# Kernel tuning notes

Hardware: AMD Instinct MI355X
Metric: run time of the kernel (lower is better)

Reference implementation:

```python
import jax, jax.numpy as jnp
import numpy as np


def setup_inputs() -> dict:
    key = jax.random.key(0)
    ks = jax.random.split(key, 5)
    B, T, C, HS = 8, 2048, 1024, 64
    return {
        "x_q": jax.random.normal(ks[0], (B, T, C), dtype=jnp.float32),
        "x_kv": jax.random.normal(ks[1], (B, T, C), dtype=jnp.float32),
        "Wq": jax.random.normal(ks[2], (C, HS), dtype=jnp.float32) * (C ** -0.5),
        "Wk": jax.random.normal(ks[3], (C, HS), dtype=jnp.float32) * (C ** -0.5),
        "Wv": jax.random.normal(ks[4], (C, HS), dtype=jnp.float32) * (C ** -0.5),
    }


def reference(x_q, x_kv, Wq, Wk, Wv):
    # x_q, x_kv: [B, T, C]; W*: [C, HS]
    B, T, C = x_q.shape
    q = jnp.einsum("btc,ch->bth", x_q, Wq)   # [B, T, HS]
    k = jnp.einsum("btc,ch->bth", x_kv, Wk)  # [B, T, HS]
    v = jnp.einsum("btc,ch->bth", x_kv, Wv)  # [B, T, HS]
    # NOTE: original scales by d_model**-0.5 (C), not head_size**-0.5
    wei = jnp.einsum("bqh,bkh->bqk", q, k) * (C ** -0.5)  # [B, T, T]
    causal = jnp.tril(jnp.ones((T, T), dtype=bool))
    wei = jnp.where(causal, wei, -jnp.inf)
    wei = jax.nn.softmax(wei, axis=-1)
    out = jnp.einsum("bqk,bkh->bqh", wei, v)  # [B, T, HS]
    return out
```

## Files before the change

### kernel.cpp

```cpp
#include <hip/hip_runtime.h>

typedef __bf16 bf16_t;
typedef __bf16 bf16x8 __attribute__((ext_vector_type(8)));
typedef float f32x4 __attribute__((ext_vector_type(4)));
typedef unsigned short u16x4 __attribute__((ext_vector_type(4)));

#define B_ 8
#define T_ 2048
#define C_ 1024
#define HS_ 64

#define MFMA __builtin_amdgcn_mfma_f32_16x16x32_bf16

__device__ __forceinline__ float fast_exp2(float x) {
#if __has_builtin(__builtin_amdgcn_exp2f)
  return __builtin_amdgcn_exp2f(x);
#else
  return exp2f(x);
#endif
}

__global__ __launch_bounds__(256) void repack_w(
    const float* __restrict__ Wq, const float* __restrict__ Wk,
    const float* __restrict__ Wv, bf16_t* __restrict__ pq,
    bf16_t* __restrict__ pk, bf16_t* __restrict__ pv) {
  const float* W = (blockIdx.y == 0) ? Wq : ((blockIdx.y == 1) ? Wk : Wv);
  bf16_t* P = (blockIdx.y == 0) ? pq : ((blockIdx.y == 1) ? pk : pv);
  int t = blockIdx.x * 256 + threadIdx.x;
  int lane = t & 63, nt = (t >> 6) & 3, kc = t >> 8;
  int quad = lane >> 4, ln = lane & 15;
  bf16x8 v;
#pragma unroll
  for (int j = 0; j < 8; ++j)
    v[j] = (bf16_t)W[(kc * 32 + quad * 8 + j) * HS_ + nt * 16 + ln];
  *(bf16x8*)(P + (size_t)t * 8) = v;
}

__global__ __launch_bounds__(512) void proj_mfma(
    const float* __restrict__ xq, const float* __restrict__ xkv,
    const bf16_t* __restrict__ pq, const bf16_t* __restrict__ pk,
    const bf16_t* __restrict__ pv, bf16_t* __restrict__ q,
    bf16_t* __restrict__ k, bf16_t* __restrict__ vT) {
  __shared__ float r0[4][16][66];
  __shared__ float r1[4][16][66];

  const int rt = blockIdx.x;
  const bool is_kv = (blockIdx.y != 0);
  const int wv = threadIdx.x >> 6, lane = threadIdx.x & 63;
  const int wr = wv & 3, kh = wv >> 2;
  const int quad = lane >> 4, ln = lane & 15;
  const int m0 = rt * 64 + wr * 16;
  const float* x = is_kv ? xkv : xq;
  const bf16_t* p0 = is_kv ? pk : pq;

  f32x4 acc0[4], acc1[4];
#pragma unroll
  for (int nt = 0; nt < 4; ++nt) {
    acc0[nt] = (f32x4){0.f, 0.f, 0.f, 0.f};
    acc1[nt] = (f32x4){0.f, 0.f, 0.f, 0.f};
  }

  for (int kc = kh * 16; kc < kh * 16 + 16; kc += 4) {
    f32x4 lo[4], hi[4];
#pragma unroll
    for (int u = 0; u < 4; ++u) {
      const float* xf = x + (size_t)(m0 + ln) * C_ + (kc + u) * 32 + quad * 8;
      lo[u] = *(const f32x4*)xf;
      hi[u] = *(const f32x4*)(xf + 4);
    }
#pragma unroll
    for (int u = 0; u < 4; ++u) {
      bf16x8 a;
#pragma unroll
      for (int j = 0; j < 4; ++j) {
        a[j] = (bf16_t)lo[u][j];
        a[4 + j] = (bf16_t)hi[u][j];
      }
#pragma unroll
      for (int nt = 0; nt < 4; ++nt) {
        bf16x8 b =
            *(const bf16x8*)(p0 + ((size_t)((kc + u) * 4 + nt) * 64 + lane) * 8);
        acc0[nt] = MFMA(a, b, acc0[nt], 0, 0, 0);
      }
      if (is_kv) {
#pragma unroll
        for (int nt = 0; nt < 4; ++nt) {
          bf16x8 b =
              *(const bf16x8*)(pv + ((size_t)((kc + u) * 4 + nt) * 64 + lane) * 8);
          acc1[nt] = MFMA(a, b, acc1[nt], 0, 0, 0);
        }
      }
    }
  }

  if (kh == 1) {
#pragma unroll
    for (int nt = 0; nt < 4; ++nt)
#pragma unroll
      for (int r = 0; r < 4; ++r) {
        r0[wr][quad * 4 + r][nt * 16 + ln] = acc0[nt][r];
        if (is_kv) r1[wr][quad * 4 + r][nt * 16 + ln] = acc1[nt][r];
      }
  }
  __syncthreads();
  if (kh != 0) return;

#pragma unroll
  for (int nt = 0; nt < 4; ++nt)
#pragma unroll
    for (int r = 0; r < 4; ++r) {
      acc0[nt][r] += r0[wr][quad * 4 + r][nt * 16 + ln];
      if (is_kv) acc1[nt][r] += r1[wr][quad * 4 + r][nt * 16 + ln];
    }

  if (!is_kv) {
#pragma unroll
    for (int nt = 0; nt < 4; ++nt)
#pragma unroll
      for (int r = 0; r < 4; ++r)
        q[(size_t)(m0 + quad * 4 + r) * HS_ + nt * 16 + ln] = (bf16_t)acc0[nt][r];
  } else {
#pragma unroll
    for (int nt = 0; nt < 4; ++nt)
#pragma unroll
      for (int r = 0; r < 4; ++r)
        k[(size_t)(m0 + quad * 4 + r) * HS_ + nt * 16 + ln] = (bf16_t)acc0[nt][r];
    const int bb = m0 >> 11, t0 = m0 & (T_ - 1);
#pragma unroll
    for (int nt = 0; nt < 4; ++nt) {
      u16x4 pk4;
#pragma unroll
      for (int r = 0; r < 4; ++r) {
        bf16_t h = (bf16_t)acc1[nt][r];
        pk4[r] = *(unsigned short*)&h;
      }
      *(u16x4*)((unsigned short*)vT + ((size_t)(bb * HS_ + nt * 16 + ln)) * T_ +
                t0 + quad * 4) = pk4;
    }
  }
}

__global__ __launch_bounds__(512) void attn_mfma(
    const bf16_t* __restrict__ q, const bf16_t* __restrict__ k,
    const bf16_t* __restrict__ vT, float* __restrict__ out) {
  __shared__ bf16_t p_lds[8][16][80];
  __shared__ float o_buf[8][16][66];
  __shared__ float l_buf[8][16][17];

  const int b = blockIdx.x >> 7;
  const int gq = blockIdx.x & 127;
  const int w = threadIdx.x >> 6, lane = threadIdx.x & 63;
  const int quad = lane >> 4, ln = lane & 15;
  const int qr0 = gq * 16;
  const size_t bt = (size_t)b * T_;
  const int td = gq >> 2;

  bf16x8 aq[2];
#pragma unroll
  for (int hc = 0; hc < 2; ++hc)
    aq[hc] = *(const bf16x8*)(q + (bt + qr0 + ln) * HS_ + hc * 32 + quad * 8);

  f32x4 o_acc[4];
  float l_part[4] = {0.f, 0.f, 0.f, 0.f};
#pragma unroll
  for (int nt = 0; nt < 4; ++nt) o_acc[nt] = (f32x4){0.f, 0.f, 0.f, 0.f};
  const float scl = 0.03125f * 1.44269504088896340736f;

  for (int t = w; t <= td; t += 8) {
    const int kr0 = t * 64;

    f32x4 s[4];
#pragma unroll
    for (int nt = 0; nt < 4; ++nt) s[nt] = (f32x4){0.f, 0.f, 0.f, 0.f};
#pragma unroll
    for (int hc = 0; hc < 2; ++hc)
#pragma unroll
      for (int nt = 0; nt < 4; ++nt) {
        bf16x8 bk = *(const bf16x8*)(k + (bt + kr0 + nt * 16 + ln) * HS_ +
                                     hc * 32 + quad * 8);
        s[nt] = MFMA(aq[hc], bk, s[nt], 0, 0, 0);
      }

    const bool diag = (t == td);
#pragma unroll
    for (int nt = 0; nt < 4; ++nt)
#pragma unroll
      for (int r = 0; r < 4; ++r) {
        float e = fast_exp2(s[nt][r] * scl);
        if (diag && (kr0 + nt * 16 + ln > qr0 + quad * 4 + r)) e = 0.f;
        l_part[r] += e;
        p_lds[w][quad * 4 + r][nt * 16 + ln] = (bf16_t)e;
      }

#pragma unroll
    for (int kc = 0; kc < 2; ++kc) {
      bf16x8 ap = *(const bf16x8*)&p_lds[w][ln][kc * 32 + quad * 8];
#pragma unroll
      for (int nt = 0; nt < 4; ++nt) {
        bf16x8 bv = *(const bf16x8*)(vT + ((size_t)(b * HS_ + nt * 16 + ln)) * T_ +
                                     kr0 + kc * 32 + quad * 8);
        o_acc[nt] = MFMA(ap, bv, o_acc[nt], 0, 0, 0);
      }
    }
  }

#pragma unroll
  for (int nt = 0; nt < 4; ++nt)
#pragma unroll
    for (int r = 0; r < 4; ++r)
      o_buf[w][quad * 4 + r][nt * 16 + ln] = o_acc[nt][r];
#pragma unroll
  for (int r = 0; r < 4; ++r) l_buf[w][quad * 4 + r][ln] = l_part[r];
  __syncthreads();

#pragma unroll
  for (int rr = 0; rr < 2; ++rr) {
    const int row = w + rr * 8;
    float o = 0.f, lsum = 0.f;
#pragma unroll
    for (int ww = 0; ww < 8; ++ww) {
      o += o_buf[ww][row][lane];
      lsum += l_buf[ww][row][lane & 15];
    }
#pragma unroll
    for (int off = 1; off < 16; off <<= 1) lsum += __shfl_xor(lsum, off);
    out[(bt + qr0 + row) * HS_ + lane] = o / lsum;
  }
}

extern "C" void kernel_launch(void* const* d_in, const int* in_sizes, int n_in,
                              void* d_out, int out_size, void* d_ws,
                              size_t ws_size, hipStream_t stream) {
  (void)in_sizes; (void)n_in; (void)out_size; (void)ws_size;
  const float* xq = (const float*)d_in[0];
  const float* xkv = (const float*)d_in[1];
  const float* Wq = (const float*)d_in[2];
  const float* Wk = (const float*)d_in[3];
  const float* Wv = (const float*)d_in[4];
  float* out = (float*)d_out;

  char* ws = (char*)d_ws;
  bf16_t* q = (bf16_t*)ws;
  bf16_t* kk = (bf16_t*)(ws + (2u << 20));
  bf16_t* vT = (bf16_t*)(ws + (4u << 20));
  bf16_t* pq = (bf16_t*)(ws + (6u << 20));
  bf16_t* pk = (bf16_t*)(ws + (6u << 20) + (128u << 10));
  bf16_t* pv = (bf16_t*)(ws + (6u << 20) + (256u << 10));

  repack_w<<<dim3(32, 3), 256, 0, stream>>>(Wq, Wk, Wv, pq, pk, pv);
  proj_mfma<<<dim3(256, 2), 512, 0, stream>>>(xq, xkv, pq, pk, pv, q, kk, vT);
  attn_mfma<<<dim3(1024), 512, 0, stream>>>(q, kk, vT, out);
}
```

Measured before the change: 219.7 us.

## Stage projection inputs through LDS with async loads, drop K-split, pad vT stride

The projection kernel now stages 64x256 fp32 tiles of x into LDS using global_load_lds direct-to-LDS loads. Each wave covers the full K range for its 16 rows, which removes the two-wave K split and its LDS reduction plus barrier, and halves the block to 256 threads. The transposed V buffer gets a padded row stride of 2080 to reduce cache and channel aliasing in attention's vT reads, and the workspace offsets move to fit it. The trade-offs are that the loads are waited on synchronously with no double buffering, and the large LDS tile limits how many blocks fit per CU.

```diff
diff --git a/kernel.cpp b/kernel.cpp
--- a/kernel.cpp
+++ b/kernel.cpp
@@ -9,6 +9,7 @@
 #define T_ 2048
 #define C_ 1024
 #define HS_ 64
+#define VSTRIDE 2080
 
 #define MFMA __builtin_amdgcn_mfma_f32_16x16x32_bf16
 
@@ -18,6 +19,12 @@
 #else
   return exp2f(x);
 #endif
+}
+
+__device__ __forceinline__ void async_ld16(const float* gsrc, float* lds_dst) {
+  __builtin_amdgcn_global_load_lds(
+      (const __attribute__((address_space(1))) void*)gsrc,
+      (__attribute__((address_space(3))) void*)lds_dst, 16, 0, 0);
 }
 
 __global__ __launch_bounds__(256) void repack_w(
@@ -36,20 +43,19 @@
   *(bf16x8*)(P + (size_t)t * 8) = v;
 }
 
-__global__ __launch_bounds__(512) void proj_mfma(
+__global__ __launch_bounds__(256) void proj_mfma(
     const float* __restrict__ xq, const float* __restrict__ xkv,
     const bf16_t* __restrict__ pq, const bf16_t* __restrict__ pk,
     const bf16_t* __restrict__ pv, bf16_t* __restrict__ q,
     bf16_t* __restrict__ k, bf16_t* __restrict__ vT) {
-  __shared__ float r0[4][16][66];
-  __shared__ float r1[4][16][66];
+  __shared__ float Xb[64][260];
 
   const int rt = blockIdx.x;
   const bool is_kv = (blockIdx.y != 0);
-  const int wv = threadIdx.x >> 6, lane = threadIdx.x & 63;
-  const int wr = wv & 3, kh = wv >> 2;
+  const int w = threadIdx.x >> 6, lane = threadIdx.x & 63;
   const int quad = lane >> 4, ln = lane & 15;
-  const int m0 = rt * 64 + wr * 16;
+  const int m0blk = rt * 64;
+  const int m0 = m0blk + w * 16;
   const float* x = is_kv ? xkv : xq;
   const bf16_t* p0 = is_kv ? pk : pq;
 
@@ -60,58 +66,41 @@
     acc1[nt] = (f32x4){0.f, 0.f, 0.f, 0.f};
   }
 
-  for (int kc = kh * 16; kc < kh * 16 + 16; kc += 4) {
-    f32x4 lo[4], hi[4];
-#pragma unroll
-    for (int u = 0; u < 4; ++u) {
-      const float* xf = x + (size_t)(m0 + ln) * C_ + (kc + u) * 32 + quad * 8;
-      lo[u] = *(const f32x4*)xf;
-      hi[u] = *(const f32x4*)(xf + 4);
-    }
-#pragma unroll
-    for (int u = 0; u < 4; ++u) {
+  for (int c = 0; c < 4; ++c) {
+#pragma unroll
+    for (int i = 0; i < 16; ++i) {
+      const int row = w * 16 + i;
+      async_ld16(x + (size_t)(m0blk + row) * C_ + c * 256 + lane * 4,
+                 &Xb[row][0]);
+    }
+    asm volatile("s_waitcnt vmcnt(0)" ::: "memory");
+
+#pragma unroll 2
+    for (int kc2 = 0; kc2 < 8; ++kc2) {
+      const int kcg = c * 8 + kc2;
+      f32x4 xlo = *(const f32x4*)&Xb[w * 16 + ln][kc2 * 32 + quad * 8];
+      f32x4 xhi = *(const f32x4*)&Xb[w * 16 + ln][kc2 * 32 + quad * 8 + 4];
       bf16x8 a;
 #pragma unroll
       for (int j = 0; j < 4; ++j) {
-        a[j] = (bf16_t)lo[u][j];
-        a[4 + j] = (bf16_t)hi[u][j];
+        a[j] = (bf16_t)xlo[j];
+        a[4 + j] = (bf16_t)xhi[j];
       }
 #pragma unroll
       for (int nt = 0; nt < 4; ++nt) {
-        bf16x8 b =
-            *(const bf16x8*)(p0 + ((size_t)((kc + u) * 4 + nt) * 64 + lane) * 8);
+        bf16x8 b = *(const bf16x8*)(p0 + ((size_t)(kcg * 4 + nt) * 64 + lane) * 8);
         acc0[nt] = MFMA(a, b, acc0[nt], 0, 0, 0);
       }
       if (is_kv) {
 #pragma unroll
         for (int nt = 0; nt < 4; ++nt) {
-          bf16x8 b =
-              *(const bf16x8*)(pv + ((size_t)((kc + u) * 4 + nt) * 64 + lane) * 8);
+          bf16x8 b = *(const bf16x8*)(pv + ((size_t)(kcg * 4 + nt) * 64 + lane) * 8);
           acc1[nt] = MFMA(a, b, acc1[nt], 0, 0, 0);
         }
       }
     }
-  }
-
-  if (kh == 1) {
-#pragma unroll
-    for (int nt = 0; nt < 4; ++nt)
-#pragma unroll
-      for (int r = 0; r < 4; ++r) {
-        r0[wr][quad * 4 + r][nt * 16 + ln] = acc0[nt][r];
-        if (is_kv) r1[wr][quad * 4 + r][nt * 16 + ln] = acc1[nt][r];
-      }
-  }
-  __syncthreads();
-  if (kh != 0) return;
-
-#pragma unroll
-  for (int nt = 0; nt < 4; ++nt)
-#pragma unroll
-    for (int r = 0; r < 4; ++r) {
-      acc0[nt][r] += r0[wr][quad * 4 + r][nt * 16 + ln];
-      if (is_kv) acc1[nt][r] += r1[wr][quad * 4 + r][nt * 16 + ln];
-    }
+    asm volatile("" ::: "memory");
+  }
 
   if (!is_kv) {
 #pragma unroll
@@ -134,7 +123,7 @@
         bf16_t h = (bf16_t)acc1[nt][r];
         pk4[r] = *(unsigned short*)&h;
       }
-      *(u16x4*)((unsigned short*)vT + ((size_t)(bb * HS_ + nt * 16 + ln)) * T_ +
+      *(u16x4*)((unsigned short*)vT + ((size_t)(bb * HS_ + nt * 16 + ln)) * VSTRIDE +
                 t0 + quad * 4) = pk4;
     }
   }
@@ -197,7 +186,8 @@
       bf16x8 ap = *(const bf16x8*)&p_lds[w][ln][kc * 32 + quad * 8];
 #pragma unroll
       for (int nt = 0; nt < 4; ++nt) {
-        bf16x8 bv = *(const bf16x8*)(vT + ((size_t)(b * HS_ + nt * 16 + ln)) * T_ +
+        bf16x8 bv = *(const bf16x8*)(vT +
+                                     ((size_t)(b * HS_ + nt * 16 + ln)) * VSTRIDE +
                                      kr0 + kc * 32 + quad * 8);
         o_acc[nt] = MFMA(ap, bv, o_acc[nt], 0, 0, 0);
       }
@@ -243,11 +233,11 @@
   bf16_t* q = (bf16_t*)ws;
   bf16_t* kk = (bf16_t*)(ws + (2u << 20));
   bf16_t* vT = (bf16_t*)(ws + (4u << 20));
-  bf16_t* pq = (bf16_t*)(ws + (6u << 20));
-  bf16_t* pk = (bf16_t*)(ws + (6u << 20) + (128u << 10));
-  bf16_t* pv = (bf16_t*)(ws + (6u << 20) + (256u << 10));
+  bf16_t* pq = (bf16_t*)(ws + (6656u << 10));
+  bf16_t* pk = (bf16_t*)(ws + (6784u << 10));
+  bf16_t* pv = (bf16_t*)(ws + (6912u << 10));
 
   repack_w<<<dim3(32, 3), 256, 0, stream>>>(Wq, Wk, Wv, pq, pk, pv);
-  proj_mfma<<<dim3(256, 2), 512, 0, stream>>>(xq, xkv, pq, pk, pv, q, kk, vT);
+  proj_mfma<<<dim3(256, 2), 256, 0, stream>>>(xq, xkv, pq, pk, pv, q, kk, vT);
   attn_mfma<<<dim3(1024), 512, 0, stream>>>(q, kk, vT, out);
 }
```

Result: no change. 217.7 us (-0.9%).
